# Performance work log

Measured on AMD Instinct MI355X. Metric: run time of the kernel, lower is better.

The kernel has to match this reference:

```python
import jax, jax.numpy as jnp
import numpy as np

EPS = 1e-6
ALPHA = 0.1
BETA = 0.25


def setup_inputs() -> dict:
    key = jax.random.key(0)
    k1, k2, k3 = jax.random.split(key, 3)
    B, C, D = 4096, 256, 128
    x = jax.random.normal(k1, (B, D), dtype=jnp.float32)
    prev_q = jax.random.normal(k2, (B, D), dtype=jnp.float32)
    codes = jax.random.normal(k3, (1, C, D), dtype=jnp.float32)
    return {"x": x, "prev_q": prev_q, "codes": codes}


def compute_distance(x, codes):
    # x: (B, D); codes: (1, C, D) or (B, 1, D) -> (B, C) / (B, 1); metric='l2'
    return jnp.sum((x[:, None, :] - codes) ** 2, axis=-1)


def get_rotation_matrix(u, v, eps=EPS):
    # u: (B, D) normalized; v: (D,) normalized -> R: (B, D, D)
    B, D = u.shape
    uvT = u[:, :, None] * v[None, None, :]          # (B, D, D) = u v^T
    vuT = v[None, :, None] * u[:, None, :]          # (B, D, D) = v u^T
    A = uvT - vuT
    A2 = jnp.einsum('bik,bkj->bij', A, A)
    dot = jnp.einsum('bd,d->b', u, v)[:, None, None]
    I = jnp.eye(D, dtype=u.dtype)
    return I + A + A2 / (1.0 + dot + eps)


def reference(x, prev_q, codes):
    B, D = x.shape
    v = jnp.ones((D,), dtype=x.dtype) / jnp.sqrt(jnp.asarray(D, x.dtype))
    # F.normalize(prev_q, dim=-1, eps=1e-6)
    n = jnp.linalg.norm(prev_q, axis=-1, keepdims=True)
    u = prev_q / jnp.maximum(n, EPS)
    R = get_rotation_matrix(u, v)
    # x_canonical = R^T x
    x_canonical = jnp.einsum('bji,bj->bi', R, x)
    raw_distances = compute_distance(x_canonical, codes)        # (B, C)
    distances = raw_distances / D / ALPHA
    # eval path: argmin + gather
    indices = jnp.argmin(distances, axis=-1)                    # (B,)
    quantized_canonical = codes[0][indices]                     # (B, D)
    quantized = jnp.einsum('bij,bj->bi', R, quantized_canonical)
    loss_commit = compute_distance(x, jax.lax.stop_gradient(quantized)[:, None, :]).mean()
    loss_codebook = compute_distance(jax.lax.stop_gradient(x), quantized[:, None, :]).mean()
    loss = loss_commit + BETA * loss_codebook
    return quantized, indices, loss
```

## Files before the change

kernel.cpp:

```cpp
#include <hip/hip_runtime.h>

#define BD 4096
#define CD 256
#define DD 128
#define RB 16
#define TB 1024
#define SF 132

__global__ __launch_bounds__(TB) void rq_fused(
    const float* __restrict__ x,
    const float* __restrict__ pq,
    const float* __restrict__ codes,
    float* __restrict__ out)
{
    __shared__ __align__(16) char pool[CD * SF * 4
                                       + RB * DD * 4
                                       + CD * 4
                                       + RB * 4 * 4
                                       + RB * 4
                                       + RB * 2 * 8
                                       + RB * 4];
    float* code_s = (float*)pool;
    float* mbuf   = (float*)pool;
    float* xc_s   = (float*)(pool + CD * SF * 4);
    float* cn2_s  = xc_s + RB * DD;
    float* row_c  = cn2_s + CD;
    float* row_s  = row_c + RB;
    float* row_invn = row_s + RB;
    float* row_pad  = row_invn + RB;  (void)row_pad;
    int*   row_idx  = (int*)(row_invn + 2 * RB);
    float* red_v    = (float*)(row_idx + RB);
    int*   red_i    = (int*)(red_v + RB * 2);
    float* loss_s   = (float*)(red_i + RB * 2);

    const int tid  = threadIdx.x;
    const int wv   = tid >> 6;
    const int lane = tid & 63;
    const int row0 = blockIdx.x * RB;
    const float INV_SQRT_D = 0.088388347648318447f;

    const size_t growA = (size_t)(row0 + wv);
    const float2 xv = ((const float2*)(x  + growA * DD))[lane];
    const float2 pv = ((const float2*)(pq + growA * DD))[lane];

    {
        const float4* src = (const float4*)codes;
        #pragma unroll
        for (int k = 0; k < 8; k += 4) {
            const float4 t0 = src[(k + 0) * TB + tid];
            const float4 t1 = src[(k + 1) * TB + tid];
            const float4 t2 = src[(k + 2) * TB + tid];
            const float4 t3 = src[(k + 3) * TB + tid];
            int f;
            f = (k + 0) * TB + tid; *(float4*)(code_s + (f >> 5) * SF + (f & 31) * 4) = t0;
            f = (k + 1) * TB + tid; *(float4*)(code_s + (f >> 5) * SF + (f & 31) * 4) = t1;
            f = (k + 2) * TB + tid; *(float4*)(code_s + (f >> 5) * SF + (f & 31) * 4) = t2;
            f = (k + 3) * TB + tid; *(float4*)(code_s + (f >> 5) * SF + (f & 31) * 4) = t3;
        }
    }

    {
        const int r = wv;
        float s0 = pv.x * pv.x + pv.y * pv.y;
        float s1 = pv.x + pv.y;
        float s2 = xv.x + xv.y;
        float s3 = pv.x * xv.x + pv.y * xv.y;
        #pragma unroll
        for (int m = 32; m > 0; m >>= 1) {
            s0 += __shfl_xor(s0, m);
            s1 += __shfl_xor(s1, m);
            s2 += __shfl_xor(s2, m);
            s3 += __shfl_xor(s3, m);
        }
        const float invn = 1.0f / fmaxf(sqrtf(s0), 1e-6f);
        const float b = s2 * INV_SQRT_D;
        const float a = s3 * invn;
        const float c = s1 * invn * INV_SQRT_D;
        const float s = 1.0f / (1.0f + c + 1e-6f);
        const float au = -b + s * (c * b - a);
        const float av =  a + s * (c * a - b);
        float2 o;
        o.x = xv.x + au * (pv.x * invn) + av * INV_SQRT_D;
        o.y = xv.y + au * (pv.y * invn) + av * INV_SQRT_D;
        ((float2*)(xc_s + r * DD))[lane] = o;
        if (lane == 0) { row_c[r] = c; row_s[r] = s; row_invn[r] = invn; }
    }
    __syncthreads();

    {
        const int c = tid >> 2, q = tid & 3;
        const float* cp = code_s + c * SF + q * 32;
        float n2 = 0.f;
        #pragma unroll
        for (int i = 0; i < 8; ++i) {
            const float4 v = *(const float4*)(cp + i * 4);
            n2 = fmaf(v.x, v.x, n2); n2 = fmaf(v.y, v.y, n2);
            n2 = fmaf(v.z, v.z, n2); n2 = fmaf(v.w, v.w, n2);
        }
        n2 += __shfl_xor(n2, 1);
        n2 += __shfl_xor(n2, 2);
        if (q == 0) cn2_s[c] = n2;
    }
    __syncthreads();

    const int wgrp = wv & 7, half = wv >> 3;
    const int rg = wgrp & 3, ch = wgrp >> 2;
    const float* cb = code_s + (ch * 128 + lane) * SF + half * 64;
    float xreg[4];
    #pragma unroll
    for (int rr = 0; rr < 4; ++rr)
        xreg[rr] = xc_s[(rg * 4 + rr) * DD + half * 64 + lane];
    float a0 = 0.f, a1 = 0.f, a2 = 0.f, a3 = 0.f;
    float a4 = 0.f, a5 = 0.f, a6 = 0.f, a7 = 0.f;

    #define RL(rr, j) __int_as_float(__builtin_amdgcn_readlane(__float_as_int(xreg[rr]), (j)))
    #pragma unroll
    for (int i = 0; i < 16; ++i) {
        const float4 c0 = *(const float4*)(cb + i * 4);
        const float4 c1 = *(const float4*)(cb + 64 * SF + i * 4);
        const float x00 = RL(0, 4 * i + 0), x01 = RL(0, 4 * i + 1);
        const float x02 = RL(0, 4 * i + 2), x03 = RL(0, 4 * i + 3);
        const float x10 = RL(1, 4 * i + 0), x11 = RL(1, 4 * i + 1);
        const float x12 = RL(1, 4 * i + 2), x13 = RL(1, 4 * i + 3);
        const float x20 = RL(2, 4 * i + 0), x21 = RL(2, 4 * i + 1);
        const float x22 = RL(2, 4 * i + 2), x23 = RL(2, 4 * i + 3);
        const float x30 = RL(3, 4 * i + 0), x31 = RL(3, 4 * i + 1);
        const float x32 = RL(3, 4 * i + 2), x33 = RL(3, 4 * i + 3);
        a0 = fmaf(c0.x, x00, a0); a0 = fmaf(c0.y, x01, a0);
        a0 = fmaf(c0.z, x02, a0); a0 = fmaf(c0.w, x03, a0);
        a1 = fmaf(c1.x, x00, a1); a1 = fmaf(c1.y, x01, a1);
        a1 = fmaf(c1.z, x02, a1); a1 = fmaf(c1.w, x03, a1);
        a2 = fmaf(c0.x, x10, a2); a2 = fmaf(c0.y, x11, a2);
        a2 = fmaf(c0.z, x12, a2); a2 = fmaf(c0.w, x13, a2);
        a3 = fmaf(c1.x, x10, a3); a3 = fmaf(c1.y, x11, a3);
        a3 = fmaf(c1.z, x12, a3); a3 = fmaf(c1.w, x13, a3);
        a4 = fmaf(c0.x, x20, a4); a4 = fmaf(c0.y, x21, a4);
        a4 = fmaf(c0.z, x22, a4); a4 = fmaf(c0.w, x23, a4);
        a5 = fmaf(c1.x, x20, a5); a5 = fmaf(c1.y, x21, a5);
        a5 = fmaf(c1.z, x22, a5); a5 = fmaf(c1.w, x23, a5);
        a6 = fmaf(c0.x, x30, a6); a6 = fmaf(c0.y, x31, a6);
        a6 = fmaf(c0.z, x32, a6); a6 = fmaf(c0.w, x33, a6);
        a7 = fmaf(c1.x, x30, a7); a7 = fmaf(c1.y, x31, a7);
        a7 = fmaf(c1.z, x32, a7); a7 = fmaf(c1.w, x33, a7);
    }
    #undef RL

    __syncthreads();
    if (half == 1) {
        float* mb = mbuf + ((size_t)wgrp * 64 + lane) * 8;
        float4 v;
        v.x = a0; v.y = a1; v.z = a2; v.w = a3; *(float4*)(mb)     = v;
        v.x = a4; v.y = a5; v.z = a6; v.w = a7; *(float4*)(mb + 4) = v;
    }
    __syncthreads();
    if (half == 0) {
        const float* mb = mbuf + ((size_t)wgrp * 64 + lane) * 8;
        const float4 m0 = *(const float4*)(mb);
        const float4 m1 = *(const float4*)(mb + 4);
        a0 += m0.x; a1 += m0.y; a2 += m0.z; a3 += m0.w;
        a4 += m1.x; a5 += m1.y; a6 += m1.z; a7 += m1.w;
        const int c0i = ch * 128 + lane;
        const int c1i = c0i + 64;
        const float cn20 = cn2_s[c0i];
        const float cn21 = cn2_s[c1i];
        float bv[4]; int bi[4];
        {
            const float s00 = fmaf(-2.f, a0, cn20), s01 = fmaf(-2.f, a1, cn21);
            const float s10 = fmaf(-2.f, a2, cn20), s11 = fmaf(-2.f, a3, cn21);
            const float s20 = fmaf(-2.f, a4, cn20), s21 = fmaf(-2.f, a5, cn21);
            const float s30 = fmaf(-2.f, a6, cn20), s31 = fmaf(-2.f, a7, cn21);
            if (s01 < s00) { bv[0] = s01; bi[0] = c1i; } else { bv[0] = s00; bi[0] = c0i; }
            if (s11 < s10) { bv[1] = s11; bi[1] = c1i; } else { bv[1] = s10; bi[1] = c0i; }
            if (s21 < s20) { bv[2] = s21; bi[2] = c1i; } else { bv[2] = s20; bi[2] = c0i; }
            if (s31 < s30) { bv[3] = s31; bi[3] = c1i; } else { bv[3] = s30; bi[3] = c0i; }
        }
        #pragma unroll
        for (int m = 1; m < 64; m <<= 1) {
            #pragma unroll
            for (int rr = 0; rr < 4; ++rr) {
                const float ov = __shfl_xor(bv[rr], m);
                const int   oi = __shfl_xor(bi[rr], m);
                if (ov < bv[rr] || (ov == bv[rr] && oi < bi[rr])) { bv[rr] = ov; bi[rr] = oi; }
            }
        }
        if (lane == 0) {
            #pragma unroll
            for (int rr = 0; rr < 4; ++rr) {
                red_v[(rg * 4 + rr) * 2 + ch] = bv[rr];
                red_i[(rg * 4 + rr) * 2 + ch] = bi[rr];
            }
        }
    }
    __syncthreads();
    if (tid < RB) {
        float v0 = red_v[tid * 2]; int i0 = red_i[tid * 2];
        const float v1 = red_v[tid * 2 + 1]; const int i1 = red_i[tid * 2 + 1];
        if (v1 < v0 || (v1 == v0 && i1 < i0)) { v0 = v1; i0 = i1; }
        row_idx[tid] = i0;
        out[(size_t)BD * DD + row0 + tid] = (float)i0;
    }
    __syncthreads();

    {
        const int r = wv;
        const int qi = row_idx[r];
        const float invn = row_invn[r];
        const float c = row_c[r];
        const float s = row_s[r];
        const size_t grow = growA;
        const float2 q = ((const float2*)(codes + (size_t)qi * DD))[lane];
        float pd = pv.x * q.x + pv.y * q.y;
        float ws = q.x + q.y;
        #pragma unroll
        for (int m = 32; m > 0; m >>= 1) {
            pd += __shfl_xor(pd, m);
            ws += __shfl_xor(ws, m);
        }
        const float pp = pd * invn;
        const float w  = ws * INV_SQRT_D;
        const float bu  =  w + s * (c * w - pp);
        const float bvv = -pp + s * (c * pp - w);
        float2 o;
        o.x = q.x + bu * (pv.x * invn) + bvv * INV_SQRT_D;
        o.y = q.y + bu * (pv.y * invn) + bvv * INV_SQRT_D;
        ((float2*)(out + grow * DD))[lane] = o;

        float dx = xv.x - o.x;
        float ls = dx * dx;
        dx = xv.y - o.y;
        ls = fmaf(dx, dx, ls);
        #pragma unroll
        for (int m = 32; m > 0; m >>= 1) ls += __shfl_xor(ls, m);
        if (lane == 0) loss_s[r] = ls;
    }
    __syncthreads();
    if (tid == 0) {
        float tot = 0.f;
        #pragma unroll
        for (int r = 0; r < RB; ++r) tot += loss_s[r];
        atomicAdd(out + (size_t)BD * DD + BD, tot * (1.25f / (float)BD));
    }
}

extern "C" void kernel_launch(void* const* d_in, const int* in_sizes, int n_in,
                              void* d_out, int out_size, void* d_ws, size_t ws_size,
                              hipStream_t stream) {
    const float* xin   = (const float*)d_in[0];
    const float* prevq = (const float*)d_in[1];
    const float* codes = (const float*)d_in[2];
    float* out = (float*)d_out;
    rq_fused<<<BD / RB, TB, 0, stream>>>(xin, prevq, codes, out);
}
```

Measured before the change: 73.93 us.

## Load codebook via global_load_lds with XOR swizzle and fuse code norms into distance loop

```diff
diff --git a/kernel.cpp b/kernel.cpp
--- a/kernel.cpp
+++ b/kernel.cpp
@@ -5,7 +5,6 @@
 #define DD 128
 #define RB 16
 #define TB 1024
-#define SF 132
 
 __global__ __launch_bounds__(TB) void rq_fused(
     const float* __restrict__ x,
@@ -13,23 +12,18 @@
     const float* __restrict__ codes,
     float* __restrict__ out)
 {
-    __shared__ __align__(16) char pool[CD * SF * 4
+    __shared__ __align__(16) char pool[CD * DD * 4
                                        + RB * DD * 4
-                                       + CD * 4
-                                       + RB * 4 * 4
-                                       + RB * 4
+                                       + RB * 3 * 4
                                        + RB * 2 * 8
                                        + RB * 4];
-    float* code_s = (float*)pool;
-    float* mbuf   = (float*)pool;
-    float* xc_s   = (float*)(pool + CD * SF * 4);
-    float* cn2_s  = xc_s + RB * DD;
-    float* row_c  = cn2_s + CD;
-    float* row_s  = row_c + RB;
+    float* code_s   = (float*)pool;
+    float* mbuf     = (float*)pool;
+    float* xc_s     = (float*)(pool + CD * DD * 4);
+    float* row_c    = xc_s + RB * DD;
+    float* row_s    = row_c + RB;
     float* row_invn = row_s + RB;
-    float* row_pad  = row_invn + RB;  (void)row_pad;
-    int*   row_idx  = (int*)(row_invn + 2 * RB);
-    float* red_v    = (float*)(row_idx + RB);
+    float* red_v    = row_invn + RB;
     int*   red_i    = (int*)(red_v + RB * 2);
     float* loss_s   = (float*)(red_i + RB * 2);
 
@@ -43,20 +37,16 @@
     const float2 xv = ((const float2*)(x  + growA * DD))[lane];
     const float2 pv = ((const float2*)(pq + growA * DD))[lane];
 
-    {
-        const float4* src = (const float4*)codes;
-        #pragma unroll
-        for (int k = 0; k < 8; k += 4) {
-            const float4 t0 = src[(k + 0) * TB + tid];
-            const float4 t1 = src[(k + 1) * TB + tid];
-            const float4 t2 = src[(k + 2) * TB + tid];
-            const float4 t3 = src[(k + 3) * TB + tid];
-            int f;
-            f = (k + 0) * TB + tid; *(float4*)(code_s + (f >> 5) * SF + (f & 31) * 4) = t0;
-            f = (k + 1) * TB + tid; *(float4*)(code_s + (f >> 5) * SF + (f & 31) * 4) = t1;
-            f = (k + 2) * TB + tid; *(float4*)(code_s + (f >> 5) * SF + (f & 31) * 4) = t2;
-            f = (k + 3) * TB + tid; *(float4*)(code_s + (f >> 5) * SF + (f & 31) * 4) = t3;
-        }
+    #pragma unroll
+    for (int k = 0; k < 8; ++k) {
+        const int f0 = k * 1024 + wv * 64;
+        const int f  = f0 + lane;
+        const int c  = f >> 5, j = f & 31;
+        const int gq = c * 32 + (j ^ (c & 31));
+        __builtin_amdgcn_global_load_lds(
+            (const __attribute__((address_space(1))) void*)(codes + (size_t)gq * 4),
+            (__attribute__((address_space(3))) void*)(code_s + (size_t)f0 * 4),
+            16, 0, 0);
     }
 
     {
@@ -87,37 +77,25 @@
     }
     __syncthreads();
 
-    {
-        const int c = tid >> 2, q = tid & 3;
-        const float* cp = code_s + c * SF + q * 32;
-        float n2 = 0.f;
-        #pragma unroll
-        for (int i = 0; i < 8; ++i) {
-            const float4 v = *(const float4*)(cp + i * 4);
-            n2 = fmaf(v.x, v.x, n2); n2 = fmaf(v.y, v.y, n2);
-            n2 = fmaf(v.z, v.z, n2); n2 = fmaf(v.w, v.w, n2);
-        }
-        n2 += __shfl_xor(n2, 1);
-        n2 += __shfl_xor(n2, 2);
-        if (q == 0) cn2_s[c] = n2;
-    }
-    __syncthreads();
-
     const int wgrp = wv & 7, half = wv >> 3;
     const int rg = wgrp & 3, ch = wgrp >> 2;
-    const float* cb = code_s + (ch * 128 + lane) * SF + half * 64;
+    const int lm = lane & 31;
+    const float* cb0 = code_s + (size_t)(ch * 128 + lane) * DD;
+    const float* cb1 = cb0 + 64 * DD;
     float xreg[4];
     #pragma unroll
     for (int rr = 0; rr < 4; ++rr)
         xreg[rr] = xc_s[(rg * 4 + rr) * DD + half * 64 + lane];
     float a0 = 0.f, a1 = 0.f, a2 = 0.f, a3 = 0.f;
     float a4 = 0.f, a5 = 0.f, a6 = 0.f, a7 = 0.f;
+    float n20 = 0.f, n21 = 0.f;
 
     #define RL(rr, j) __int_as_float(__builtin_amdgcn_readlane(__float_as_int(xreg[rr]), (j)))
     #pragma unroll
     for (int i = 0; i < 16; ++i) {
-        const float4 c0 = *(const float4*)(cb + i * 4);
-        const float4 c1 = *(const float4*)(cb + 64 * SF + i * 4);
+        const int slot = ((half * 16 + i) ^ lm) * 4;
+        const float4 c0 = *(const float4*)(cb0 + slot);
+        const float4 c1 = *(const float4*)(cb1 + slot);
         const float x00 = RL(0, 4 * i + 0), x01 = RL(0, 4 * i + 1);
         const float x02 = RL(0, 4 * i + 2), x03 = RL(0, 4 * i + 3);
         const float x10 = RL(1, 4 * i + 0), x11 = RL(1, 4 * i + 1);
@@ -126,6 +104,10 @@
         const float x22 = RL(2, 4 * i + 2), x23 = RL(2, 4 * i + 3);
         const float x30 = RL(3, 4 * i + 0), x31 = RL(3, 4 * i + 1);
         const float x32 = RL(3, 4 * i + 2), x33 = RL(3, 4 * i + 3);
+        n20 = fmaf(c0.x, c0.x, n20); n20 = fmaf(c0.y, c0.y, n20);
+        n20 = fmaf(c0.z, c0.z, n20); n20 = fmaf(c0.w, c0.w, n20);
+        n21 = fmaf(c1.x, c1.x, n21); n21 = fmaf(c1.y, c1.y, n21);
+        n21 = fmaf(c1.z, c1.z, n21); n21 = fmaf(c1.w, c1.w, n21);
         a0 = fmaf(c0.x, x00, a0); a0 = fmaf(c0.y, x01, a0);
         a0 = fmaf(c0.z, x02, a0); a0 = fmaf(c0.w, x03, a0);
         a1 = fmaf(c1.x, x00, a1); a1 = fmaf(c1.y, x01, a1);
@@ -147,22 +129,24 @@
 
     __syncthreads();
     if (half == 1) {
-        float* mb = mbuf + ((size_t)wgrp * 64 + lane) * 8;
+        float* mb = mbuf + ((size_t)wgrp * 64 + lane) * 12;
         float4 v;
         v.x = a0; v.y = a1; v.z = a2; v.w = a3; *(float4*)(mb)     = v;
         v.x = a4; v.y = a5; v.z = a6; v.w = a7; *(float4*)(mb + 4) = v;
+        float2 w; w.x = n20; w.y = n21;         *(float2*)(mb + 8) = w;
     }
     __syncthreads();
     if (half == 0) {
-        const float* mb = mbuf + ((size_t)wgrp * 64 + lane) * 8;
+        const float* mb = mbuf + ((size_t)wgrp * 64 + lane) * 12;
         const float4 m0 = *(const float4*)(mb);
         const float4 m1 = *(const float4*)(mb + 4);
+        const float2 m2 = *(const float2*)(mb + 8);
         a0 += m0.x; a1 += m0.y; a2 += m0.z; a3 += m0.w;
         a4 += m1.x; a5 += m1.y; a6 += m1.z; a7 += m1.w;
+        const float cn20 = n20 + m2.x;
+        const float cn21 = n21 + m2.y;
         const int c0i = ch * 128 + lane;
         const int c1i = c0i + 64;
-        const float cn20 = cn2_s[c0i];
-        const float cn21 = cn2_s[c1i];
         float bv[4]; int bi[4];
         {
             const float s00 = fmaf(-2.f, a0, cn20), s01 = fmaf(-2.f, a1, cn21);
@@ -192,22 +176,17 @@
         }
     }
     __syncthreads();
-    if (tid < RB) {
-        float v0 = red_v[tid * 2]; int i0 = red_i[tid * 2];
-        const float v1 = red_v[tid * 2 + 1]; const int i1 = red_i[tid * 2 + 1];
-        if (v1 < v0 || (v1 == v0 && i1 < i0)) { v0 = v1; i0 = i1; }
-        row_idx[tid] = i0;
-        out[(size_t)BD * DD + row0 + tid] = (float)i0;
-    }
-    __syncthreads();
 
     {
         const int r = wv;
-        const int qi = row_idx[r];
+        const float v0 = red_v[r * 2],  v1 = red_v[r * 2 + 1];
+        const int   i0 = red_i[r * 2],  i1 = red_i[r * 2 + 1];
+        const int qi = (v1 < v0 || (v1 == v0 && i1 < i0)) ? i1 : i0;
+        if (lane == 0) out[(size_t)BD * DD + row0 + r] = (float)qi;
+
         const float invn = row_invn[r];
         const float c = row_c[r];
         const float s = row_s[r];
-        const size_t grow = growA;
         const float2 q = ((const float2*)(codes + (size_t)qi * DD))[lane];
         float pd = pv.x * q.x + pv.y * q.y;
         float ws = q.x + q.y;
@@ -223,7 +202,7 @@
         float2 o;
         o.x = q.x + bu * (pv.x * invn) + bvv * INV_SQRT_D;
         o.y = q.y + bu * (pv.y * invn) + bvv * INV_SQRT_D;
-        ((float2*)(out + grow * DD))[lane] = o;
+        ((float2*)(out + growA * DD))[lane] = o;
 
         float dx = xv.x - o.x;
         float ls = dx * dx;
```

After: 74.51 us. About the same (+0.8%).
